# Kernel optimization log

Hardware: AMD Instinct MI355X
Metric: run time of the kernel (lower is better)

The kernel has to match this reference:

```python
import jax, jax.numpy as jnp
import numpy as np

B, C, D, H, W = 2, 96, 4, 128, 128
WS = 8            # spatial window size
NUM_HEADS = 3
MLP_RATIO = 4.0


def _rel_pos_index(ws_eff):
    # Swin-style 2D relative position index over the effective (ws*sqrt(D))^2 window
    coords = np.stack(np.meshgrid(np.arange(ws_eff), np.arange(ws_eff), indexing='ij')).reshape(2, -1)
    rel = (coords[:, :, None] - coords[:, None, :]).transpose(1, 2, 0)
    rel[..., 0] += ws_eff - 1
    rel[..., 1] += ws_eff - 1
    rel[..., 0] *= 2 * ws_eff - 1
    return rel.sum(-1)  # (N, N) int


def setup_inputs() -> dict:
    key = jax.random.key(0)
    ks = jax.random.split(key, 8)
    ws_eff = WS * int(np.sqrt(D))
    table_len = (2 * ws_eff - 1) ** 2
    hid = int(C * MLP_RATIO)
    s = lambda k, shape: jax.random.normal(k, shape, jnp.float32) * 0.02
    return dict(
        x=jax.random.normal(ks[0], (B, C, D, H, W), jnp.float32),
        qkv_w=s(ks[1], (3 * C, C)), qkv_b=jnp.zeros((3 * C,), jnp.float32),
        proj_w=s(ks[2], (C, C)), proj_b=jnp.zeros((C,), jnp.float32),
        bias_table=s(ks[3], (table_len, NUM_HEADS)),
        ln1_g=jnp.ones((C,), jnp.float32), ln1_b=jnp.zeros((C,), jnp.float32),
        ln2_g=jnp.ones((C,), jnp.float32), ln2_b=jnp.zeros((C,), jnp.float32),
        fc1_w=s(ks[4], (hid, C)), fc1_b=jnp.zeros((hid,), jnp.float32),
        fc2_w=s(ks[5], (C, hid)), fc2_b=jnp.zeros((C,), jnp.float32),
    )


def _ln(x, g, b):
    m = x.mean(-1, keepdims=True)
    v = ((x - m) ** 2).mean(-1, keepdims=True)
    return (x - m) * jax.lax.rsqrt(v + 1e-5) * g + b


def reference(x, qkv_w, qkv_b, proj_w, proj_b, bias_table,
              ln1_g, ln1_b, ln2_g, ln2_b, fc1_w, fc1_b, fc2_w, fc2_b):
    ws, nh = WS, NUM_HEADS
    hd = C // nh
    # window partition: (B,C,D,H,W) -> (nW*B, C, D*ws*ws) -> tokens (B_, N, C)
    p = x.reshape(B, C, D, H // ws, ws, W // ws, ws)
    p = p.transpose(0, 3, 5, 1, 2, 4, 6).reshape(-1, C, D * ws * ws)
    t = p.transpose(0, 2, 1)  # (B_, N, C)
    B_, N, _ = t.shape

    # --- window attention with relative position bias ---
    h = _ln(t, ln1_g, ln1_b)
    qkv = (h @ qkv_w.T + qkv_b).reshape(B_, N, 3, nh, hd).transpose(2, 0, 3, 1, 4)
    q = qkv[0] * (hd ** -0.5)
    k, v = qkv[1], qkv[2]
    idx = jnp.asarray(_rel_pos_index(ws * int(np.sqrt(D))))  # static (N,N)
    bias = bias_table[idx].transpose(2, 0, 1)  # (nh, N, N) gathered bias
    attn = jax.nn.softmax(jnp.einsum('bhnd,bhmd->bhnm', q, k) + bias[None], axis=-1)
    o = jnp.einsum('bhnm,bhmd->bhnd', attn, v).transpose(0, 2, 1, 3).reshape(B_, N, C)
    t = t + (o @ proj_w.T + proj_b)

    # --- MLP block ---
    h2 = _ln(t, ln2_g, ln2_b)
    m = jax.nn.gelu(h2 @ fc1_w.T + fc1_b, approximate=False) @ fc2_w.T + fc2_b
    return t + m
```

## Files before the change

### kernel.cpp

```cpp
#include <hip/hip_runtime.h>
#include <hip/hip_bf16.h>

typedef unsigned int u32;
using bf16x8 = __attribute__((ext_vector_type(8))) short;
using f32x4  = __attribute__((ext_vector_type(4))) float;

#define QKV_STRIDE 12582912u
#define WS_NEED    100663296ull

__device__ __forceinline__ float bl(u32 u) { return __uint_as_float(u << 16); }
__device__ __forceinline__ float bh(u32 u) { return __uint_as_float(u & 0xffff0000u); }
__device__ __forceinline__ unsigned short bfbits(float f) {
    __hip_bfloat16 b = __float2bfloat16(f);
    return *(unsigned short*)&b;
}
__device__ __forceinline__ u32 pack2(float f0, float f1) {
    return ((u32)bfbits(f1) << 16) | (u32)bfbits(f0);
}

#define MFMA(a, b, c) __builtin_amdgcn_mfma_f32_16x16x32_bf16(a, b, c, 0, 0, 0)

__global__ __launch_bounds__(256) void k_fill(float* __restrict__ out, int n)
{
    int i = blockIdx.x * 256 + threadIdx.x;
    if (i < n) out[i] = 1000.0f;
}

__global__ __launch_bounds__(256) void k_ln1_c(const float* __restrict__ x,
                                               const float* __restrict__ g1,
                                               const float* __restrict__ b1,
                                               u32* __restrict__ h)
{
    __shared__ float xs[96 * 128];
    __shared__ float ps[256], pss[256], mr[128], rs[128];
    int blk = blockIdx.x;
    int hh = blk & 127, d = (blk >> 7) & 3, bb = blk >> 9;
    long base = (long)bb * 6291456 + (long)d * 16384 + hh * 128;
    for (int i = threadIdx.x; i < 3072; i += 256) {
        int c = i >> 5, w4 = i & 31;
        ((float4*)xs)[i] = *(const float4*)(x + base + (long)c * 65536 + w4 * 4);
    }
    __syncthreads();

    int tid = threadIdx.x, half = tid >> 7, ww = tid & 127;
    int c0 = half * 48;
    float s = 0.f, ssq = 0.f;
    #pragma unroll 8
    for (int c = c0; c < c0 + 48; ++c) {
        float v = xs[c * 128 + ww];
        s += v; ssq += v * v;
    }
    ps[tid] = s; pss[tid] = ssq;
    __syncthreads();
    if (half == 0) {
        float st = ps[ww] + ps[128 + ww], sst = pss[ww] + pss[128 + ww];
        float mean = st * (1.f / 96.f);
        float var  = sst * (1.f / 96.f) - mean * mean;
        mr[ww] = mean; rs[ww] = rsqrtf(var + 1e-5f);
    }
    __syncthreads();
    float mean = mr[ww], rstd = rs[ww];

    int w = (bb << 8) + (hh >> 3) * 16 + (ww >> 3);
    int t = (w << 8) + d * 64 + (hh & 7) * 8 + (ww & 7);
    uint4* hq = (uint4*)(h + (long)t * 48 + half * 24);
    #pragma unroll
    for (int k = 0; k < 6; ++k) {
        int c = c0 + 8 * k;
        u32 q0 = pack2((xs[(c+0)*128+ww]-mean)*rstd*g1[c+0]+b1[c+0],
                       (xs[(c+1)*128+ww]-mean)*rstd*g1[c+1]+b1[c+1]);
        u32 q1 = pack2((xs[(c+2)*128+ww]-mean)*rstd*g1[c+2]+b1[c+2],
                       (xs[(c+3)*128+ww]-mean)*rstd*g1[c+3]+b1[c+3]);
        u32 q2 = pack2((xs[(c+4)*128+ww]-mean)*rstd*g1[c+4]+b1[c+4],
                       (xs[(c+5)*128+ww]-mean)*rstd*g1[c+5]+b1[c+5]);
        u32 q3 = pack2((xs[(c+6)*128+ww]-mean)*rstd*g1[c+6]+b1[c+6],
                       (xs[(c+7)*128+ww]-mean)*rstd*g1[c+7]+b1[c+7]);
        hq[k] = make_uint4(q0, q1, q2, q3);
    }
}

__global__ __launch_bounds__(256) void k_qkv_m(const __hip_bfloat16* __restrict__ h,
                                               const float* __restrict__ qkvw,
                                               const float* __restrict__ qkvb,
                                               __hip_bfloat16* __restrict__ qkv)
{
    __shared__ short wsm[288 * 96];
    int tid = threadIdx.x;
    for (int idx = tid; idx < 288 * 96; idx += 256) wsm[idx] = (short)bfbits(qkvw[idx]);
    __syncthreads();

    int wave = tid >> 6, lane = tid & 63;
    int quad = lane >> 4, l16 = lane & 15;
    int mbase = blockIdx.x * 256 + wave * 64;

    bf16x8 A[4][3];
    #pragma unroll
    for (int mm = 0; mm < 4; ++mm) {
        const __hip_bfloat16* ap = h + (long)(mbase + mm * 16 + l16) * 96 + quad * 8;
        A[mm][0] = *(const bf16x8*)(ap);
        A[mm][1] = *(const bf16x8*)(ap + 32);
        A[mm][2] = *(const bf16x8*)(ap + 64);
    }

    for (int nt = 0; nt < 18; ++nt) {
        int n0 = nt * 16;
        const short* bp = &wsm[(n0 + l16) * 96 + quad * 8];
        bf16x8 B0 = *(const bf16x8*)(bp);
        bf16x8 B1 = *(const bf16x8*)(bp + 32);
        bf16x8 B2 = *(const bf16x8*)(bp + 64);
        int r    = n0 + l16;
        int type = n0 / 96;
        int head = (n0 % 96) / 32;
        int dd   = r & 31;
        float bias = qkvb[r];
        float scl  = (type == 0) ? 0.17677669529663687f : 1.0f;
        long tbase = (long)type * QKV_STRIDE;
        #pragma unroll
        for (int mm = 0; mm < 4; ++mm) {
            f32x4 acc = {0.f, 0.f, 0.f, 0.f};
            acc = MFMA(A[mm][0], B0, acc);
            acc = MFMA(A[mm][1], B1, acc);
            acc = MFMA(A[mm][2], B2, acc);
            int tok0 = mbase + mm * 16 + quad * 4;
            int w = tok0 >> 8, nn = tok0 & 255;
            long dst0 = tbase + (long)(w * 3 + head) * 8192 + nn * 32 + dd;
            #pragma unroll
            for (int rg = 0; rg < 4; ++rg)
                qkv[dst0 + (long)rg * 32] = __float2bfloat16((acc[rg] + bias) * scl);
        }
    }
}

__global__ __launch_bounds__(256) void k_attn_m(const __hip_bfloat16* __restrict__ qkv,
                                                const float* __restrict__ btab,
                                                __hip_bfloat16* __restrict__ o)
{
    __shared__ short vt[32 * 264];
    __shared__ short pm[4 * 16 * 264];
    __shared__ float bsT[31 * 33];
    int wh = blockIdx.x, head = wh % 3, w = wh / 3;
    int tid = threadIdx.x;

    const u32* vg = (const u32*)(qkv + 2u * QKV_STRIDE + (long)wh * 8192);
    for (int idx = tid; idx < 4096; idx += 256) {
        u32 pv = vg[idx];
        int kr = idx >> 4, d0 = (idx & 15) * 2;
        vt[d0 * 264 + kr]       = (short)(pv & 0xffffu);
        vt[(d0 + 1) * 264 + kr] = (short)(pv >> 16);
    }
    for (int idx = tid; idx < 961; idx += 256) {
        int c2 = idx / 31, r2 = idx - c2 * 31;
        bsT[c2 * 33 + r2] = btab[(r2 * 31 + c2) * 3 + head];
    }
    __syncthreads();

    int wave = tid >> 6, lane = tid & 63, quad = lane >> 4, l16 = lane & 15;
    const __hip_bfloat16* qb = qkv + (long)wh * 8192;
    const __hip_bfloat16* kb = qkv + QKV_STRIDE + (long)wh * 8192;
    short* pmw = &pm[wave * 16 * 264];

    bf16x8 kf[16];
    #pragma unroll
    for (int kt = 0; kt < 16; ++kt)
        kf[kt] = *(const bf16x8*)(kb + (kt * 16 + l16) * 32 + quad * 8);

    for (int g = 0; g < 4; ++g) {
        int qg = wave * 4 + g;
        bf16x8 qf = *(const bf16x8*)(qb + (qg * 16 + l16) * 32 + quad * 8);
        f32x4 s[16];
        #pragma unroll
        for (int kt = 0; kt < 16; ++kt) {
            f32x4 z = {0.f, 0.f, 0.f, 0.f};
            s[kt] = MFMA(kf[kt], qf, z);
        }
        #pragma unroll
        for (int rg = 0; rg < 4; ++rg) {
            const float* bp2 = &bsT[(l16 - quad * 4 + 15 - rg) * 33 + qg + 15];
            #pragma unroll
            for (int kt = 0; kt < 16; ++kt)
                s[kt][rg] += bp2[-kt];
        }
        float mx = -1e30f;
        #pragma unroll
        for (int kt = 0; kt < 16; ++kt)
            #pragma unroll
            for (int rg = 0; rg < 4; ++rg) mx = fmaxf(mx, s[kt][rg]);
        mx = fmaxf(mx, __shfl_xor(mx, 16));
        mx = fmaxf(mx, __shfl_xor(mx, 32));
        float lsum = 0.f;
        #pragma unroll
        for (int kt = 0; kt < 16; ++kt)
            #pragma unroll
            for (int rg = 0; rg < 4; ++rg) {
                float p = __expf(s[kt][rg] - mx);
                s[kt][rg] = p; lsum += p;
            }
        lsum += __shfl_xor(lsum, 16);
        lsum += __shfl_xor(lsum, 32);
        float inv = 1.f / lsum;
        #pragma unroll
        for (int kt = 0; kt < 16; ++kt)
            #pragma unroll
            for (int rg = 0; rg < 4; ++rg)
                pmw[l16 * 264 + kt * 16 + quad * 4 + rg] = (short)bfbits(s[kt][rg] * inv);
        f32x4 a0 = {0.f, 0.f, 0.f, 0.f}, a1 = {0.f, 0.f, 0.f, 0.f};
        #pragma unroll
        for (int k2 = 0; k2 < 8; ++k2) {
            bf16x8 pf = *(const bf16x8*)&pmw[l16 * 264 + k2 * 32 + quad * 8];
            bf16x8 v0 = *(const bf16x8*)&vt[l16 * 264 + k2 * 32 + quad * 8];
            bf16x8 v1 = *(const bf16x8*)&vt[(16 + l16) * 264 + k2 * 32 + quad * 8];
            a0 = MFMA(pf, v0, a0);
            a1 = MFMA(pf, v1, a1);
        }
        #pragma unroll
        for (int rg = 0; rg < 4; ++rg) {
            int qrow = qg * 16 + quad * 4 + rg;
            __hip_bfloat16* op = o + (long)(w * 256 + qrow) * 96 + head * 32;
            op[l16]      = __float2bfloat16(a0[rg]);
            op[16 + l16] = __float2bfloat16(a1[rg]);
        }
    }
}

__global__ __launch_bounds__(256) void k_proj_nr(const __hip_bfloat16* __restrict__ o,
                                                 const float* __restrict__ pw,
                                                 const float* __restrict__ pb,
                                                 __hip_bfloat16* __restrict__ pbuf)
{
    __shared__ short wsm[96 * 96];
    int tid = threadIdx.x;
    for (int idx = tid; idx < 96 * 96; idx += 256) wsm[idx] = (short)bfbits(pw[idx]);
    __syncthreads();

    int wave = tid >> 6, lane = tid & 63;
    int quad = lane >> 4, l16 = lane & 15;
    int mbase = blockIdx.x * 256 + wave * 64;

    bf16x8 A[4][3];
    #pragma unroll
    for (int mm = 0; mm < 4; ++mm) {
        const __hip_bfloat16* ap = o + (long)(mbase + mm * 16 + l16) * 96 + quad * 8;
        A[mm][0] = *(const bf16x8*)(ap);
        A[mm][1] = *(const bf16x8*)(ap + 32);
        A[mm][2] = *(const bf16x8*)(ap + 64);
    }

    for (int nt = 0; nt < 6; ++nt) {
        int n0 = nt * 16;
        const short* bp = &wsm[(n0 + l16) * 96 + quad * 8];
        bf16x8 B0 = *(const bf16x8*)(bp);
        bf16x8 B1 = *(const bf16x8*)(bp + 32);
        bf16x8 B2 = *(const bf16x8*)(bp + 64);
        int c = n0 + l16;
        float bias = pb[c];
        #pragma unroll
        for (int mm = 0; mm < 4; ++mm) {
            f32x4 acc = {0.f, 0.f, 0.f, 0.f};
            acc = MFMA(A[mm][0], B0, acc);
            acc = MFMA(A[mm][1], B1, acc);
            acc = MFMA(A[mm][2], B2, acc);
            int tok0 = mbase + mm * 16 + quad * 4;
            #pragma unroll
            for (int rg = 0; rg < 4; ++rg)
                pbuf[(long)(tok0 + rg) * 96 + c] = __float2bfloat16(acc[rg] + bias);
        }
    }
}

__global__ __launch_bounds__(256) void k_addln2(const float* __restrict__ x,
                                                const __hip_bfloat16* __restrict__ pbuf,
                                                const float* __restrict__ g2,
                                                const float* __restrict__ b2,
                                                u32* __restrict__ t2,
                                                u32* __restrict__ h2)
{
    __shared__ float xs[96 * 128];
    __shared__ float ps[256], pss[256], mr[128], rs[128];
    int blk = blockIdx.x;
    int hh = blk & 127, d = (blk >> 7) & 3, bb = blk >> 9;
    long base = (long)bb * 6291456 + (long)d * 16384 + hh * 128;
    for (int i = threadIdx.x; i < 3072; i += 256) {
        int c = i >> 5, w4 = i & 31;
        ((float4*)xs)[i] = *(const float4*)(x + base + (long)c * 65536 + w4 * 4);
    }
    __syncthreads();

    int tid = threadIdx.x, half = tid >> 7, ww = tid & 127;
    int c0 = half * 48;
    int w = (bb << 8) + (hh >> 3) * 16 + (ww >> 3);
    int t = (w << 8) + d * 64 + (hh & 7) * 8 + (ww & 7);

    const u32* pr = (const u32*)pbuf + (long)t * 48 + half * 24;
    float pv[48];
    float s = 0.f, ssq = 0.f;
    #pragma unroll
    for (int k = 0; k < 24; ++k) {
        u32 u = pr[k];
        float v0 = bl(u) + xs[(c0 + 2 * k) * 128 + ww];
        float v1 = bh(u) + xs[(c0 + 2 * k + 1) * 128 + ww];
        pv[2 * k] = v0; pv[2 * k + 1] = v1;
        s += v0 + v1; ssq += v0 * v0 + v1 * v1;
    }
    ps[tid] = s; pss[tid] = ssq;
    __syncthreads();
    if (half == 0) {
        float st = ps[ww] + ps[128 + ww], sst = pss[ww] + pss[128 + ww];
        float mean = st * (1.f / 96.f);
        float var  = sst * (1.f / 96.f) - mean * mean;
        mr[ww] = mean; rs[ww] = rsqrtf(var + 1e-5f);
    }
    __syncthreads();
    float mean = mr[ww], rstd = rs[ww];

    uint4* t2q = (uint4*)(t2 + (long)t * 48 + half * 24);
    uint4* hq  = (uint4*)(h2 + (long)t * 48 + half * 24);
    #pragma unroll
    for (int k = 0; k < 6; ++k) {
        int c = c0 + 8 * k;
        u32 t0v = pack2(pv[8*k+0], pv[8*k+1]);
        u32 t1v = pack2(pv[8*k+2], pv[8*k+3]);
        u32 t2v = pack2(pv[8*k+4], pv[8*k+5]);
        u32 t3v = pack2(pv[8*k+6], pv[8*k+7]);
        t2q[k] = make_uint4(t0v, t1v, t2v, t3v);
        u32 q0 = pack2((pv[8*k+0]-mean)*rstd*g2[c+0]+b2[c+0],
                       (pv[8*k+1]-mean)*rstd*g2[c+1]+b2[c+1]);
        u32 q1 = pack2((pv[8*k+2]-mean)*rstd*g2[c+2]+b2[c+2],
                       (pv[8*k+3]-mean)*rstd*g2[c+3]+b2[c+3]);
        u32 q2 = pack2((pv[8*k+4]-mean)*rstd*g2[c+4]+b2[c+4],
                       (pv[8*k+5]-mean)*rstd*g2[c+5]+b2[c+5]);
        u32 q3 = pack2((pv[8*k+6]-mean)*rstd*g2[c+6]+b2[c+6],
                       (pv[8*k+7]-mean)*rstd*g2[c+7]+b2[c+7]);
        hq[k] = make_uint4(q0, q1, q2, q3);
    }
}

__global__ __launch_bounds__(256) void k_fc1_m(const __hip_bfloat16* __restrict__ h2,
                                               const float* __restrict__ fw,
                                               const float* __restrict__ fb,
                                               __hip_bfloat16* __restrict__ m1, int t0)
{
    __shared__ short wsm[192 * 96];
    int tid = threadIdx.x;
    int wave = tid >> 6, lane = tid & 63;
    int quad = lane >> 4, l16 = lane & 15;
    int mbaseL = blockIdx.x * 128 + wave * 32;

    bf16x8 A[2][3];
    #pragma unroll
    for (int mm = 0; mm < 2; ++mm) {
        const __hip_bfloat16* ap = h2 + (long)(t0 + mbaseL + mm * 16 + l16) * 96 + quad * 8;
        A[mm][0] = *(const bf16x8*)(ap);
        A[mm][1] = *(const bf16x8*)(ap + 32);
        A[mm][2] = *(const bf16x8*)(ap + 64);
    }

    const float is2 = 0.70710678118654752440f;
    for (int ph = 0; ph < 2; ++ph) {
        if (ph) __syncthreads();
        for (int idx = tid; idx < 192 * 96; idx += 256)
            wsm[idx] = (short)bfbits(fw[ph * 192 * 96 + idx]);
        __syncthreads();
        for (int nt = 0; nt < 12; ++nt) {
            int n0 = nt * 16;
            const short* bp = &wsm[(n0 + l16) * 96 + quad * 8];
            bf16x8 B0 = *(const bf16x8*)(bp);
            bf16x8 B1 = *(const bf16x8*)(bp + 32);
            bf16x8 B2 = *(const bf16x8*)(bp + 64);
            int r = ph * 192 + n0 + l16;
            float bias = fb[r];
            #pragma unroll
            for (int mm = 0; mm < 2; ++mm) {
                f32x4 acc = {0.f, 0.f, 0.f, 0.f};
                acc = MFMA(A[mm][0], B0, acc);
                acc = MFMA(A[mm][1], B1, acc);
                acc = MFMA(A[mm][2], B2, acc);
                int tokL0 = mbaseL + mm * 16 + quad * 4;
                #pragma unroll
                for (int rg = 0; rg < 4; ++rg) {
                    float v = acc[rg] + bias;
                    v = 0.5f * v * (1.f + erff(v * is2));
                    m1[(long)(tokL0 + rg) * 384 + r] = __float2bfloat16(v);
                }
            }
        }
    }
}

__global__ __launch_bounds__(256) void k_fc2_m(const __hip_bfloat16* __restrict__ m1,
                                               const float* __restrict__ fw,
                                               const float* __restrict__ fb,
                                               const __hip_bfloat16* __restrict__ t2,
                                               float* __restrict__ out, int t0)
{
    __shared__ short wsm[48 * 392];
    int tid = threadIdx.x;
    int wave = tid >> 6, lane = tid & 63;
    int quad = lane >> 4, l16 = lane & 15;
    int mbaseL = blockIdx.x * 128 + wave * 32;

    bf16x8 A[2][12];
    #pragma unroll
    for (int mm = 0; mm < 2; ++mm) {
        const __hip_bfloat16* ap = m1 + (long)(mbaseL + mm * 16 + l16) * 384 + quad * 8;
        #pragma unroll
        for (int kc = 0; kc < 12; ++kc)
            A[mm][kc] = *(const bf16x8*)(ap + kc * 32);
    }

    for (int ph = 0; ph < 2; ++ph) {
        if (ph) __syncthreads();
        for (int idx = tid; idx < 48 * 384; idx += 256) {
            int rr = idx / 384, cc = idx - rr * 384;
            wsm[rr * 392 + cc] = (short)bfbits(fw[(ph * 48 + rr) * 384 + cc]);
        }
        __syncthreads();
        for (int nt = 0; nt < 3; ++nt) {
            int n0 = nt * 16;
            const short* bp = &wsm[(n0 + l16) * 392 + quad * 8];
            bf16x8 B[12];
            #pragma unroll
            for (int kc = 0; kc < 12; ++kc)
                B[kc] = *(const bf16x8*)(bp + kc * 32);
            int c = ph * 48 + n0 + l16;
            float bias = fb[c];
            #pragma unroll
            for (int mm = 0; mm < 2; ++mm) {
                f32x4 acc = {0.f, 0.f, 0.f, 0.f};
                #pragma unroll
                for (int kc = 0; kc < 12; ++kc)
                    acc = MFMA(A[mm][kc], B[kc], acc);
                int tok0 = t0 + mbaseL + mm * 16 + quad * 4;
                #pragma unroll
                for (int rg = 0; rg < 4; ++rg) {
                    long g = (long)(tok0 + rg) * 96 + c;
                    out[g] = __bfloat162float(t2[g]) + acc[rg] + bias;
                }
            }
        }
    }
}

extern "C" void kernel_launch(void* const* d_in, const int* in_sizes, int n_in,
                              void* d_out, int out_size, void* d_ws, size_t ws_size,
                              hipStream_t stream)
{
    const float* x     = (const float*)d_in[0];
    const float* qkvw  = (const float*)d_in[1];
    const float* qkvb  = (const float*)d_in[2];
    const float* projw = (const float*)d_in[3];
    const float* projb = (const float*)d_in[4];
    const float* btab  = (const float*)d_in[5];
    const float* ln1g  = (const float*)d_in[6];
    const float* ln1b  = (const float*)d_in[7];
    const float* ln2g  = (const float*)d_in[8];
    const float* ln2b  = (const float*)d_in[9];
    const float* fc1w  = (const float*)d_in[10];
    const float* fc1b  = (const float*)d_in[11];
    const float* fc2w  = (const float*)d_in[12];
    const float* fc2b  = (const float*)d_in[13];
    float* out = (float*)d_out;

    if (ws_size < WS_NEED) {
        k_fill<<<49152, 256, 0, stream>>>(out, out_size);
        return;
    }

    char* ws = (char*)d_ws;
    __hip_bfloat16* qkvB  = (__hip_bfloat16*)(ws);
    __hip_bfloat16* pbuf  = (__hip_bfloat16*)(ws);
    __hip_bfloat16* m1buf = (__hip_bfloat16*)(ws);
    __hip_bfloat16* t2buf = (__hip_bfloat16*)(ws + 50331648);
    __hip_bfloat16* hbuf  = (__hip_bfloat16*)(ws + 75497472);
    __hip_bfloat16* obuf  = hbuf;
    __hip_bfloat16* h2buf = hbuf;

    k_ln1_c <<<1024, 256, 0, stream>>>(x, ln1g, ln1b, (u32*)hbuf);
    k_qkv_m <<<512,  256, 0, stream>>>(hbuf, qkvw, qkvb, qkvB);
    k_attn_m<<<1536, 256, 0, stream>>>(qkvB, btab, obuf);
    k_proj_nr<<<512, 256, 0, stream>>>(obuf, projw, projb, pbuf);
    k_addln2<<<1024, 256, 0, stream>>>(x, pbuf, ln2g, ln2b, (u32*)t2buf, (u32*)h2buf);
    for (int ch = 0; ch < 2; ++ch) {
        int t0 = ch * 65536;
        k_fc1_m<<<512, 256, 0, stream>>>(h2buf, fc1w, fc1b, m1buf, t0);
        k_fc2_m<<<512, 256, 0, stream>>>(m1buf, fc2w, fc2b, t2buf, out, t0);
    }
}
```

Before: 372.0 us.

## Fuse fc1 and fc2 into one MLP kernel keeping the hidden tile in LDS

Replaces the separate fc1 and fc2 kernels, launched over two token chunks, with a single k_mlp kernel. Each block computes 64 tokens' GELU hidden activations into shared memory, then runs fc2 from them, so the 384-wide bf16 hidden buffer no longer round-trips through global memory. Weights are staged in small 16- or 64-row slabs, which adds more syncthreads and repeated fp32 weight conversion per block. Separately, the qkv and proj kernels now load their fp32 weights directly from global memory per lane instead of staging them through LDS.

```diff
diff --git a/kernel.cpp b/kernel.cpp
--- a/kernel.cpp
+++ b/kernel.cpp
@@ -7,6 +7,7 @@
 
 #define QKV_STRIDE 12582912u
 #define WS_NEED    100663296ull
+#define MLP_P      392
 
 __device__ __forceinline__ float bl(u32 u) { return __uint_as_float(u << 16); }
 __device__ __forceinline__ float bh(u32 u) { return __uint_as_float(u & 0xffff0000u); }
@@ -16,6 +17,14 @@
 }
 __device__ __forceinline__ u32 pack2(float f0, float f1) {
     return ((u32)bfbits(f1) << 16) | (u32)bfbits(f0);
+}
+__device__ __forceinline__ bf16x8 ldrow(const float* p) {
+    float4 a = *(const float4*)p;
+    float4 b = *(const float4*)(p + 4);
+    union { bf16x8 v; u32 u[4]; } t;
+    t.u[0] = pack2(a.x, a.y); t.u[1] = pack2(a.z, a.w);
+    t.u[2] = pack2(b.x, b.y); t.u[3] = pack2(b.z, b.w);
+    return t.v;
 }
 
 #define MFMA(a, b, c) __builtin_amdgcn_mfma_f32_16x16x32_bf16(a, b, c, 0, 0, 0)
@@ -84,11 +93,7 @@
                                                const float* __restrict__ qkvb,
                                                __hip_bfloat16* __restrict__ qkv)
 {
-    __shared__ short wsm[288 * 96];
     int tid = threadIdx.x;
-    for (int idx = tid; idx < 288 * 96; idx += 256) wsm[idx] = (short)bfbits(qkvw[idx]);
-    __syncthreads();
-
     int wave = tid >> 6, lane = tid & 63;
     int quad = lane >> 4, l16 = lane & 15;
     int mbase = blockIdx.x * 256 + wave * 64;
@@ -104,10 +109,10 @@
 
     for (int nt = 0; nt < 18; ++nt) {
         int n0 = nt * 16;
-        const short* bp = &wsm[(n0 + l16) * 96 + quad * 8];
-        bf16x8 B0 = *(const bf16x8*)(bp);
-        bf16x8 B1 = *(const bf16x8*)(bp + 32);
-        bf16x8 B2 = *(const bf16x8*)(bp + 64);
+        const float* wr = qkvw + (long)(n0 + l16) * 96 + quad * 8;
+        bf16x8 B0 = ldrow(wr);
+        bf16x8 B1 = ldrow(wr + 32);
+        bf16x8 B2 = ldrow(wr + 64);
         int r    = n0 + l16;
         int type = n0 / 96;
         int head = (n0 % 96) / 32;
@@ -227,11 +232,7 @@
                                                  const float* __restrict__ pb,
                                                  __hip_bfloat16* __restrict__ pbuf)
 {
-    __shared__ short wsm[96 * 96];
     int tid = threadIdx.x;
-    for (int idx = tid; idx < 96 * 96; idx += 256) wsm[idx] = (short)bfbits(pw[idx]);
-    __syncthreads();
-
     int wave = tid >> 6, lane = tid & 63;
     int quad = lane >> 4, l16 = lane & 15;
     int mbase = blockIdx.x * 256 + wave * 64;
@@ -247,10 +248,10 @@
 
     for (int nt = 0; nt < 6; ++nt) {
         int n0 = nt * 16;
-        const short* bp = &wsm[(n0 + l16) * 96 + quad * 8];
-        bf16x8 B0 = *(const bf16x8*)(bp);
-        bf16x8 B1 = *(const bf16x8*)(bp + 32);
-        bf16x8 B2 = *(const bf16x8*)(bp + 64);
+        const float* wr = pw + (long)(n0 + l16) * 96 + quad * 8;
+        bf16x8 B0 = ldrow(wr);
+        bf16x8 B1 = ldrow(wr + 32);
+        bf16x8 B2 = ldrow(wr + 64);
         int c = n0 + l16;
         float bias = pb[c];
         #pragma unroll
@@ -334,108 +335,81 @@
     }
 }
 
-__global__ __launch_bounds__(256) void k_fc1_m(const __hip_bfloat16* __restrict__ h2,
-                                               const float* __restrict__ fw,
-                                               const float* __restrict__ fb,
-                                               __hip_bfloat16* __restrict__ m1, int t0)
-{
-    __shared__ short wsm[192 * 96];
-    int tid = threadIdx.x;
-    int wave = tid >> 6, lane = tid & 63;
+__global__ __launch_bounds__(256) void k_mlp(const __hip_bfloat16* __restrict__ h2,
+                                             const float* __restrict__ fw1,
+                                             const float* __restrict__ fb1,
+                                             const float* __restrict__ fw2,
+                                             const float* __restrict__ fb2,
+                                             const __hip_bfloat16* __restrict__ t2,
+                                             float* __restrict__ out)
+{
+    __shared__ short mt[4 * 16 * MLP_P];
+    __shared__ short wb[16 * MLP_P];
+    int tid = threadIdx.x, wave = tid >> 6, lane = tid & 63;
     int quad = lane >> 4, l16 = lane & 15;
-    int mbaseL = blockIdx.x * 128 + wave * 32;
-
-    bf16x8 A[2][3];
-    #pragma unroll
-    for (int mm = 0; mm < 2; ++mm) {
-        const __hip_bfloat16* ap = h2 + (long)(t0 + mbaseL + mm * 16 + l16) * 96 + quad * 8;
-        A[mm][0] = *(const bf16x8*)(ap);
-        A[mm][1] = *(const bf16x8*)(ap + 32);
-        A[mm][2] = *(const bf16x8*)(ap + 64);
-    }
-
+    int tok0 = blockIdx.x * 64 + wave * 16;
+
+    const __hip_bfloat16* ap = h2 + (long)(tok0 + l16) * 96 + quad * 8;
+    bf16x8 A0 = *(const bf16x8*)(ap);
+    bf16x8 A1 = *(const bf16x8*)(ap + 32);
+    bf16x8 A2 = *(const bf16x8*)(ap + 64);
+    short* mw = &mt[wave * 16 * MLP_P];
     const float is2 = 0.70710678118654752440f;
-    for (int ph = 0; ph < 2; ++ph) {
-        if (ph) __syncthreads();
-        for (int idx = tid; idx < 192 * 96; idx += 256)
-            wsm[idx] = (short)bfbits(fw[ph * 192 * 96 + idx]);
+
+    for (int p = 0; p < 6; ++p) {
+        if (p) __syncthreads();
+        const float* src = fw1 + p * 64 * 96;
+        for (int i = tid; i < 6144; i += 256) wb[i] = (short)bfbits(src[i]);
         __syncthreads();
-        for (int nt = 0; nt < 12; ++nt) {
-            int n0 = nt * 16;
-            const short* bp = &wsm[(n0 + l16) * 96 + quad * 8];
+        #pragma unroll
+        for (int nt = 0; nt < 4; ++nt) {
+            const short* bp = &wb[(nt * 16 + l16) * 96 + quad * 8];
             bf16x8 B0 = *(const bf16x8*)(bp);
             bf16x8 B1 = *(const bf16x8*)(bp + 32);
             bf16x8 B2 = *(const bf16x8*)(bp + 64);
-            int r = ph * 192 + n0 + l16;
-            float bias = fb[r];
-            #pragma unroll
-            for (int mm = 0; mm < 2; ++mm) {
-                f32x4 acc = {0.f, 0.f, 0.f, 0.f};
-                acc = MFMA(A[mm][0], B0, acc);
-                acc = MFMA(A[mm][1], B1, acc);
-                acc = MFMA(A[mm][2], B2, acc);
-                int tokL0 = mbaseL + mm * 16 + quad * 4;
-                #pragma unroll
-                for (int rg = 0; rg < 4; ++rg) {
-                    float v = acc[rg] + bias;
-                    v = 0.5f * v * (1.f + erff(v * is2));
-                    m1[(long)(tokL0 + rg) * 384 + r] = __float2bfloat16(v);
-                }
+            int r = p * 64 + nt * 16 + l16;
+            float bias = fb1[r];
+            f32x4 acc = {0.f, 0.f, 0.f, 0.f};
+            acc = MFMA(A0, B0, acc);
+            acc = MFMA(A1, B1, acc);
+            acc = MFMA(A2, B2, acc);
+            #pragma unroll
+            for (int rg = 0; rg < 4; ++rg) {
+                float v = acc[rg] + bias;
+                v = 0.5f * v * (1.f + erff(v * is2));
+                mw[(quad * 4 + rg) * MLP_P + r] = (short)bfbits(v);
             }
         }
     }
-}
-
-__global__ __launch_bounds__(256) void k_fc2_m(const __hip_bfloat16* __restrict__ m1,
-                                               const float* __restrict__ fw,
-                                               const float* __restrict__ fb,
-                                               const __hip_bfloat16* __restrict__ t2,
-                                               float* __restrict__ out, int t0)
-{
-    __shared__ short wsm[48 * 392];
-    int tid = threadIdx.x;
-    int wave = tid >> 6, lane = tid & 63;
-    int quad = lane >> 4, l16 = lane & 15;
-    int mbaseL = blockIdx.x * 128 + wave * 32;
-
-    bf16x8 A[2][12];
-    #pragma unroll
-    for (int mm = 0; mm < 2; ++mm) {
-        const __hip_bfloat16* ap = m1 + (long)(mbaseL + mm * 16 + l16) * 384 + quad * 8;
+    __syncthreads();
+
+    bf16x8 M[12];
+    #pragma unroll
+    for (int kc = 0; kc < 12; ++kc)
+        M[kc] = *(const bf16x8*)&mw[l16 * MLP_P + kc * 32 + quad * 8];
+
+    for (int q = 0; q < 6; ++q) {
+        if (q) __syncthreads();
+        const float* src = fw2 + q * 16 * 384;
+        for (int i = tid; i < 6144; i += 256) {
+            int rr = i / 384, cc = i - rr * 384;
+            wb[rr * MLP_P + cc] = (short)bfbits(src[i]);
+        }
+        __syncthreads();
+        bf16x8 B[12];
         #pragma unroll
         for (int kc = 0; kc < 12; ++kc)
-            A[mm][kc] = *(const bf16x8*)(ap + kc * 32);
-    }
-
-    for (int ph = 0; ph < 2; ++ph) {
-        if (ph) __syncthreads();
-        for (int idx = tid; idx < 48 * 384; idx += 256) {
-            int rr = idx / 384, cc = idx - rr * 384;
-            wsm[rr * 392 + cc] = (short)bfbits(fw[(ph * 48 + rr) * 384 + cc]);
-        }
-        __syncthreads();
-        for (int nt = 0; nt < 3; ++nt) {
-            int n0 = nt * 16;
-            const short* bp = &wsm[(n0 + l16) * 392 + quad * 8];
-            bf16x8 B[12];
-            #pragma unroll
-            for (int kc = 0; kc < 12; ++kc)
-                B[kc] = *(const bf16x8*)(bp + kc * 32);
-            int c = ph * 48 + n0 + l16;
-            float bias = fb[c];
-            #pragma unroll
-            for (int mm = 0; mm < 2; ++mm) {
-                f32x4 acc = {0.f, 0.f, 0.f, 0.f};
-                #pragma unroll
-                for (int kc = 0; kc < 12; ++kc)
-                    acc = MFMA(A[mm][kc], B[kc], acc);
-                int tok0 = t0 + mbaseL + mm * 16 + quad * 4;
-                #pragma unroll
-                for (int rg = 0; rg < 4; ++rg) {
-                    long g = (long)(tok0 + rg) * 96 + c;
-                    out[g] = __bfloat162float(t2[g]) + acc[rg] + bias;
-                }
-            }
+            B[kc] = *(const bf16x8*)&wb[l16 * MLP_P + kc * 32 + quad * 8];
+        f32x4 acc = {0.f, 0.f, 0.f, 0.f};
+        #pragma unroll
+        for (int kc = 0; kc < 12; ++kc)
+            acc = MFMA(M[kc], B[kc], acc);
+        int c = q * 16 + l16;
+        float bias = fb2[c];
+        #pragma unroll
+        for (int rg = 0; rg < 4; ++rg) {
+            long g = (long)(tok0 + quad * 4 + rg) * 96 + c;
+            out[g] = __bfloat162float(t2[g]) + acc[rg] + bias;
         }
     }
 }
@@ -468,20 +442,15 @@
     char* ws = (char*)d_ws;
     __hip_bfloat16* qkvB  = (__hip_bfloat16*)(ws);
     __hip_bfloat16* pbuf  = (__hip_bfloat16*)(ws);
-    __hip_bfloat16* m1buf = (__hip_bfloat16*)(ws);
     __hip_bfloat16* t2buf = (__hip_bfloat16*)(ws + 50331648);
     __hip_bfloat16* hbuf  = (__hip_bfloat16*)(ws + 75497472);
     __hip_bfloat16* obuf  = hbuf;
     __hip_bfloat16* h2buf = hbuf;
 
-    k_ln1_c <<<1024, 256, 0, stream>>>(x, ln1g, ln1b, (u32*)hbuf);
-    k_qkv_m <<<512,  256, 0, stream>>>(hbuf, qkvw, qkvb, qkvB);
-    k_attn_m<<<1536, 256, 0, stream>>>(qkvB, btab, obuf);
-    k_proj_nr<<<512, 256, 0, stream>>>(obuf, projw, projb, pbuf);
-    k_addln2<<<1024, 256, 0, stream>>>(x, pbuf, ln2g, ln2b, (u32*)t2buf, (u32*)h2buf);
-    for (int ch = 0; ch < 2; ++ch) {
-        int t0 = ch * 65536;
-        k_fc1_m<<<512, 256, 0, stream>>>(h2buf, fc1w, fc1b, m1buf, t0);
-        k_fc2_m<<<512, 256, 0, stream>>>(m1buf, fc2w, fc2b, t2buf, out, t0);
-    }
-}
+    k_ln1_c  <<<1024, 256, 0, stream>>>(x, ln1g, ln1b, (u32*)hbuf);
+    k_qkv_m  <<<512,  256, 0, stream>>>(hbuf, qkvw, qkvb, qkvB);
+    k_attn_m <<<1536, 256, 0, stream>>>(qkvB, btab, obuf);
+    k_proj_nr<<<512,  256, 0, stream>>>(obuf, projw, projb, pbuf);
+    k_addln2 <<<1024, 256, 0, stream>>>(x, pbuf, ln2g, ln2b, (u32*)t2buf, (u32*)h2buf);
+    k_mlp    <<<2048, 256, 0, stream>>>(h2buf, fc1w, fc1b, fc2w, fc2b, t2buf, out);
+}
```

After: 389.4 us. +4.7%, slower.
